# Kernel tuning notes

Measured on AMD Instinct MI355X. Metric: run time of the kernel, lower is better.

The kernel has to match this reference:

```python
import jax, jax.numpy as jnp
import numpy as np

DIM = 2048
NUM_HEADS = 8
HEAD_DIM = DIM // NUM_HEADS
BATCH = 16384
EPS = 1e-5


def setup_inputs() -> dict:
    key = jax.random.key(0)
    ks = jax.random.split(key, 10)
    s = 1.0 / np.sqrt(DIM)
    inp = {
        "x": jax.random.normal(ks[0], (BATCH, 1, DIM), dtype=jnp.float32),
        "w_q": jax.random.uniform(ks[1], (DIM, DIM), jnp.float32, -s, s),
        "b_q": jax.random.uniform(ks[2], (DIM,), jnp.float32, -s, s),
        "w_k": jax.random.uniform(ks[3], (DIM, DIM), jnp.float32, -s, s),
        "b_k": jax.random.uniform(ks[4], (DIM,), jnp.float32, -s, s),
        "w_v": jax.random.uniform(ks[5], (DIM, DIM), jnp.float32, -s, s),
        "b_v": jax.random.uniform(ks[6], (DIM,), jnp.float32, -s, s),
        "w_o": jax.random.uniform(ks[7], (DIM, DIM), jnp.float32, -s, s),
        "b_o": jax.random.uniform(ks[8], (DIM,), jnp.float32, -s, s),
        "ln_gamma": jnp.ones((DIM,), jnp.float32),
        "ln_beta": jnp.zeros((DIM,), jnp.float32),
    }
    return inp


def _layer_norm(x, gamma, beta):
    mean = jnp.mean(x, axis=-1, keepdims=True)
    var = jnp.mean(jnp.square(x - mean), axis=-1, keepdims=True)
    return (x - mean) * jax.lax.rsqrt(var + EPS) * gamma + beta


def reference(x, w_q, b_q, w_k, b_k, w_v, b_v, w_o, b_o, ln_gamma, ln_beta):
    # x: (B, 1, D). Dropout is identity (eval mode).
    residual = x
    h = _layer_norm(x, ln_gamma, ln_beta)
    q = h @ w_q.T + b_q  # (B, 1, D)
    k = h @ w_k.T + b_k
    v = h @ w_v.T + b_v
    B = x.shape[0]
    # (B, H, 1, hd)
    qh = q.reshape(B, 1, NUM_HEADS, HEAD_DIM).transpose(0, 2, 1, 3)
    kh = k.reshape(B, 1, NUM_HEADS, HEAD_DIM).transpose(0, 2, 1, 3)
    vh = v.reshape(B, 1, NUM_HEADS, HEAD_DIM).transpose(0, 2, 1, 3)
    scale = HEAD_DIM ** -0.5
    # (B, H, 1, 1); with seq_len=1 softmax is trivially 1, but keep the math faithful
    scores = jnp.einsum("bhqd,bhkd->bhqk", qh, kh) * scale
    probs = jax.nn.softmax(scores, axis=-1)
    attn = jnp.einsum("bhqk,bhkd->bhqd", probs, vh)  # (B, H, 1, hd)
    attn = attn.transpose(0, 2, 1, 3).reshape(B, 1, DIM)
    out = attn @ w_o.T + b_o
    out = out + residual
    return out[:, 0, :]  # squeeze seq dim -> (B, D)
```

## Files before the change

### kernel.cpp

```cpp
#include <hip/hip_runtime.h>
#include <hip/hip_bf16.h>
#include <cstdint>

#define D_MODEL 2048
#define N_BATCH 16384

typedef __attribute__((ext_vector_type(8))) __bf16 bf16x8;
typedef __attribute__((ext_vector_type(4))) float f32x4;

__device__ __forceinline__ unsigned short f2bf(float f) {
    unsigned int u = __builtin_bit_cast(unsigned int, f);
    u += 0x7fffu + ((u >> 16) & 1u);
    return (unsigned short)(u >> 16);
}

__global__ __launch_bounds__(256) void prep_kernel(
    const float* __restrict__ w_v, const float* __restrict__ w_o,
    const float* __restrict__ b_v, const float* __restrict__ b_o,
    unsigned short* __restrict__ wvT, unsigned short* __restrict__ woB,
    float* __restrict__ b_c)
{
    __shared__ float tile[32][33];
    const int b = blockIdx.x;
    const int t = threadIdx.x;
    if (b < 4096) {
        const int nb = 64;
        const int k0 = (b % nb) * 32;
        const int j0 = (b / nb) * 32;
        const int tx = t & 31, ty0 = t >> 5;
        #pragma unroll
        for (int i = 0; i < 32; i += 8) {
            int j = ty0 + i;
            tile[j][tx] = w_v[(long)(j0 + j) * D_MODEL + k0 + tx];
        }
        __syncthreads();
        #pragma unroll
        for (int i = 0; i < 32; i += 8) {
            int kk = ty0 + i;
            wvT[(long)(k0 + kk) * D_MODEL + j0 + tx] = f2bf(tile[tx][kk]);
        }
    } else if (b < 6144) {
        long i = ((long)(b - 4096) * 256 + t) * 8;
        const float4* in4 = reinterpret_cast<const float4*>(w_o + i);
        float4 a = in4[0], bb = in4[1];
        union { unsigned short u[8]; uint4 v; } o;
        o.u[0] = f2bf(a.x); o.u[1] = f2bf(a.y); o.u[2] = f2bf(a.z); o.u[3] = f2bf(a.w);
        o.u[4] = f2bf(bb.x); o.u[5] = f2bf(bb.y); o.u[6] = f2bf(bb.z); o.u[7] = f2bf(bb.w);
        *reinterpret_cast<uint4*>(woB + i) = o.v;
    } else {
        const int n = b - 6144;
        const float4* w4 = reinterpret_cast<const float4*>(w_o + (long)n * D_MODEL);
        const float4* v4 = reinterpret_cast<const float4*>(b_v);
        float4 a = w4[t], bb = w4[256 + t], va = v4[t], vb = v4[256 + t];
        float s = a.x*va.x + a.y*va.y + a.z*va.z + a.w*va.w
                + bb.x*vb.x + bb.y*vb.y + bb.z*vb.z + bb.w*vb.w;
        #pragma unroll
        for (int off = 32; off; off >>= 1) s += __shfl_xor(s, off);
        float* red = &tile[0][0];
        const int lane = t & 63, wid = t >> 6;
        if (lane == 0) red[wid] = s;
        __syncthreads();
        if (t == 0) b_c[n] = red[0] + red[1] + red[2] + red[3] + b_o[n];
    }
}

__global__ __launch_bounds__(256) void lnwc_kernel(
    const unsigned short* __restrict__ A, const unsigned short* __restrict__ B,
    unsigned short* __restrict__ C,
    const float* __restrict__ x, const float* __restrict__ gamma,
    const float* __restrict__ beta, unsigned short* __restrict__ h)
{
    __shared__ __align__(16) unsigned short Alds[128 * 32];
    __shared__ __align__(16) unsigned short Blds[128 * 32];
    const int t = threadIdx.x;

    if (blockIdx.x < 256) {
        const int K = D_MODEL, N = D_MODEL;
        int wg = blockIdx.x;
        wg = (wg & 7) * 32 + (wg >> 3);
        const int bm = wg >> 4, bn = wg & 15;

        const int lane = t & 63, wid = t >> 6;
        const int wr = wid >> 1, wc = wid & 1;

        f32x4 acc[4][4];
        #pragma unroll
        for (int i = 0; i < 4; i++)
            #pragma unroll
            for (int j = 0; j < 4; j++) acc[i][j] = (f32x4){0.f, 0.f, 0.f, 0.f};

        const long Abase = (long)bm * 128 * K;
        const long Bbase = (long)bn * 128 * K;
        const int ci0 = wid * 64 + lane;
        const int ci1 = 256 + ci0;
        const int r0 = ci0 >> 2, c0 = (ci0 & 3) * 8;
        const int r1 = ci1 >> 2, c1 = (ci1 & 3) * 8;

        const int arow = wr * 64 + (lane & 15);
        const int brow = wc * 64 + (lane & 15);
        const int koff = (lane >> 4) * 8;

        for (int k0 = 0; k0 < K; k0 += 32) {
            __builtin_amdgcn_global_load_lds(
                (const __attribute__((address_space(1))) void*)(A + Abase + (long)r0 * K + k0 + c0),
                (__attribute__((address_space(3))) void*)(Alds + wid * 512), 16, 0, 0);
            __builtin_amdgcn_global_load_lds(
                (const __attribute__((address_space(1))) void*)(A + Abase + (long)r1 * K + k0 + c1),
                (__attribute__((address_space(3))) void*)(Alds + 2048 + wid * 512), 16, 0, 0);
            __builtin_amdgcn_global_load_lds(
                (const __attribute__((address_space(1))) void*)(B + Bbase + (long)r0 * K + k0 + c0),
                (__attribute__((address_space(3))) void*)(Blds + wid * 512), 16, 0, 0);
            __builtin_amdgcn_global_load_lds(
                (const __attribute__((address_space(1))) void*)(B + Bbase + (long)r1 * K + k0 + c1),
                (__attribute__((address_space(3))) void*)(Blds + 2048 + wid * 512), 16, 0, 0);
            __syncthreads();

            bf16x8 af[4], bfr[4];
            #pragma unroll
            for (int m = 0; m < 4; m++)
                af[m] = *reinterpret_cast<const bf16x8*>(&Alds[(arow + m * 16) * 32 + koff]);
            #pragma unroll
            for (int n = 0; n < 4; n++)
                bfr[n] = *reinterpret_cast<const bf16x8*>(&Blds[(brow + n * 16) * 32 + koff]);
            #pragma unroll
            for (int m = 0; m < 4; m++)
                #pragma unroll
                for (int n = 0; n < 4; n++)
                    acc[m][n] = __builtin_amdgcn_mfma_f32_16x16x32_bf16(af[m], bfr[n], acc[m][n], 0, 0, 0);
            __syncthreads();
        }

        const int crow0 = bm * 128 + wr * 64 + ((lane >> 4) << 2);
        const int ccol0 = bn * 128 + wc * 64 + (lane & 15);
        #pragma unroll
        for (int m = 0; m < 4; m++)
            #pragma unroll
            for (int j = 0; j < 4; j++) {
                const long r = crow0 + m * 16 + j;
                #pragma unroll
                for (int n = 0; n < 4; n++)
                    C[r * N + ccol0 + n * 16] = f2bf(acc[m][n][j]);
            }
    } else {
        const int row = blockIdx.x - 256;
        const float4* x4 = reinterpret_cast<const float4*>(x + (long)row * D_MODEL);
        float4 a = x4[t];
        float4 b = x4[256 + t];
        float s  = a.x + a.y + a.z + a.w + b.x + b.y + b.z + b.w;
        float ss = a.x*a.x + a.y*a.y + a.z*a.z + a.w*a.w
                 + b.x*b.x + b.y*b.y + b.z*b.z + b.w*b.w;
        #pragma unroll
        for (int off = 32; off; off >>= 1) {
            s  += __shfl_xor(s, off);
            ss += __shfl_xor(ss, off);
        }
        float* red = reinterpret_cast<float*>(Alds);
        const int lane = t & 63, wid = t >> 6;
        if (lane == 0) { red[wid*2] = s; red[wid*2+1] = ss; }
        __syncthreads();
        s  = red[0] + red[2] + red[4] + red[6];
        ss = red[1] + red[3] + red[5] + red[7];
        const float mean = s * (1.0f / D_MODEL);
        const float var  = ss * (1.0f / D_MODEL) - mean * mean;
        const float inv  = rsqrtf(var + 1e-5f);

        const float4* g4  = reinterpret_cast<const float4*>(gamma);
        const float4* be4 = reinterpret_cast<const float4*>(beta);
        ushort4* h4 = reinterpret_cast<ushort4*>(h + (long)row * D_MODEL);
        {
            float4 g = g4[t], be = be4[t];
            ushort4 o;
            o.x = f2bf((a.x - mean) * inv * g.x + be.x);
            o.y = f2bf((a.y - mean) * inv * g.y + be.y);
            o.z = f2bf((a.z - mean) * inv * g.z + be.z);
            o.w = f2bf((a.w - mean) * inv * g.w + be.w);
            h4[t] = o;
        }
        {
            float4 g = g4[256 + t], be = be4[256 + t];
            ushort4 o;
            o.x = f2bf((b.x - mean) * inv * g.x + be.x);
            o.y = f2bf((b.y - mean) * inv * g.y + be.y);
            o.z = f2bf((b.z - mean) * inv * g.z + be.z);
            o.w = f2bf((b.w - mean) * inv * g.w + be.w);
            h4[256 + t] = o;
        }
    }
}

#define GLL(src, dst) __builtin_amdgcn_global_load_lds( \
    (const __attribute__((address_space(1))) void*)(src), \
    (__attribute__((address_space(3))) void*)(dst), 16, 0, 0)
#define WAITV4() do { asm volatile("s_waitcnt vmcnt(4)" ::: "memory"); \
                      __builtin_amdgcn_sched_barrier(0); } while (0)
#define WAITV0() do { asm volatile("s_waitcnt vmcnt(0)" ::: "memory"); \
                      __builtin_amdgcn_sched_barrier(0); } while (0)

__global__ __launch_bounds__(512, 2) void gemm_bt_8ph(
    const unsigned short* __restrict__ A, const unsigned short* __restrict__ B,
    float* __restrict__ C, const float* __restrict__ bias,
    const float* __restrict__ resid, int M, int N, int K)
{
    __shared__ __align__(16) char ldsb[131072];

    const int nBN = N >> 8;
    int wg = blockIdx.x;
    const int cpx = gridDim.x >> 3;
    wg = (wg & 7) * cpx + (wg >> 3);
    const int bm = wg / nBN, bn = wg % nBN;

    const int t = threadIdx.x;
    const int lane = t & 63, wid = t >> 6;
    const int wr = wid >> 2;
    const int wc = wid & 3;

    const long Kl = K;
    const int tr = t >> 3;
    const int c8 = ((t & 7) ^ (tr & 7)) * 8;
    const unsigned short* As = A + (long)(bm * 256 + tr) * Kl + c8;
    const unsigned short* Bs = B + (long)(bn * 256 + tr) * Kl + c8;

#define ST_A(buf, half, kcol) do { \
    const unsigned short* s_ = As + (half) * 128 * Kl + (kcol); \
    char* d_ = ldsb + (buf) * 65536 + (half) * 16384 + t * 16; \
    GLL(s_, d_); GLL(s_ + 64 * Kl, d_ + 8192); } while (0)
#define ST_B(buf, half, kcol) do { \
    const unsigned short* s_ = Bs + (half) * 128 * Kl + (kcol); \
    char* d_ = ldsb + (buf) * 65536 + 32768 + (half) * 16384 + t * 16; \
    GLL(s_, d_); GLL(s_ + 64 * Kl, d_ + 8192); } while (0)

    const int l15 = lane & 15, l4 = lane >> 4;
    const int swz0 = ((l4)     ^ (l15 & 7)) << 4;
    const int swz1 = ((4 + l4) ^ (l15 & 7)) << 4;
    const int aOff = wr * 16384 + l15 * 128;
    const int bOff = 32768 + (wc >> 1) * 16384 + ((wc & 1) * 64 + l15) * 128;

#define LDV(off) (*reinterpret_cast<const bf16x8*>(ldsb + (off)))
#define RD_A(buf, mh) do { \
    _Pragma("unroll") for (int mi = 0; mi < 4; ++mi) \
        af[mi][0] = LDV((buf) * 65536 + aOff + ((mh) * 4 + mi) * 2048 + swz0); \
    _Pragma("unroll") for (int mi = 0; mi < 4; ++mi) \
        af[mi][1] = LDV((buf) * 65536 + aOff + ((mh) * 4 + mi) * 2048 + swz1); } while (0)
#define RD_B0(buf) do { \
    _Pragma("unroll") for (int nj = 0; nj < 2; ++nj) \
        b0[nj][0] = LDV((buf) * 65536 + bOff + nj * 2048 + swz0); \
    _Pragma("unroll") for (int nj = 0; nj < 2; ++nj) \
        b0[nj][1] = LDV((buf) * 65536 + bOff + nj * 2048 + swz1); } while (0)
#define RD_B1(buf) do { \
    _Pragma("unroll") for (int nj = 0; nj < 2; ++nj) \
        b1[nj][0] = LDV((buf) * 65536 + bOff + (2 + nj) * 2048 + swz0); \
    _Pragma("unroll") for (int nj = 0; nj < 2; ++nj) \
        b1[nj][1] = LDV((buf) * 65536 + bOff + (2 + nj) * 2048 + swz1); } while (0)

#define MMQ(mh, nh, BQ) do { \
    __builtin_amdgcn_s_setprio(1); \
    _Pragma("unroll") for (int kk = 0; kk < 2; ++kk) \
    _Pragma("unroll") for (int mi = 0; mi < 4; ++mi) \
    _Pragma("unroll") for (int nj = 0; nj < 2; ++nj) \
        acc[(mh) * 4 + mi][(nh) * 2 + nj] = __builtin_amdgcn_mfma_f32_16x16x32_bf16( \
            af[mi][kk], BQ[nj][kk], acc[(mh) * 4 + mi][(nh) * 2 + nj], 0, 0, 0); \
    __builtin_amdgcn_s_setprio(0); } while (0)
#define ENDP() __builtin_amdgcn_s_barrier()

    bf16x8 af[4][2], b0[2][2], b1[2][2];
    f32x4 acc[8][4];
    #pragma unroll
    for (int i = 0; i < 8; i++)
        #pragma unroll
        for (int j = 0; j < 4; j++) acc[i][j] = (f32x4){0.f, 0.f, 0.f, 0.f};

    const int NI = K >> 7;

    ST_A(0, 0, 0); ST_A(0, 1, 0); ST_B(0, 0, 0); ST_B(0, 1, 0);
    ST_B(1, 0, 64); ST_A(1, 0, 64);
    WAITV4();
    __builtin_amdgcn_s_barrier();

    for (int i = 0; i < NI; ++i) {
        const int kcA1 = (i << 7) + 64;
        const int kcN0 = (i << 7) + 128;
        const int kcN1 = (i << 7) + 192;
        const bool more = (i + 1 < NI);

        RD_A(0, 0); RD_B0(0);
        ST_A(1, 1, kcA1);
        MMQ(0, 0, b0); ENDP();
        RD_B1(0);
        ST_B(1, 1, kcA1);
        MMQ(0, 1, b1); ENDP();
        RD_A(0, 1);
        if (more) ST_B(0, 0, kcN0);
        MMQ(1, 0, b0); ENDP();
        if (more) ST_A(0, 0, kcN0);
        MMQ(1, 1, b1);
        if (more) { WAITV4(); } else { WAITV0(); }
        ENDP();
        RD_A(1, 0); RD_B0(1);
        if (more) ST_A(0, 1, kcN0);
        MMQ(0, 0, b0); ENDP();
        RD_B1(1);
        if (more) ST_B(0, 1, kcN0);
        MMQ(0, 1, b1); ENDP();
        RD_A(1, 1);
        if (more) ST_B(1, 0, kcN1);
        MMQ(1, 0, b0); ENDP();
        if (more) ST_A(1, 0, kcN1);
        MMQ(1, 1, b1);
        if (more) { WAITV4(); }
        ENDP();
    }
#undef ST_A
#undef ST_B
#undef RD_A
#undef RD_B0
#undef RD_B1
#undef MMQ
#undef ENDP
#undef LDV

    const int crow0 = bm * 256 + wr * 128 + l4 * 4;
    const int ccol0 = bn * 256 + wc * 64 + l15;
    #pragma unroll
    for (int m = 0; m < 8; m++)
        #pragma unroll
        for (int j = 0; j < 4; j++) {
            const long r = crow0 + m * 16 + j;
            float* crow = C + r * N;
            const float* rrow = resid + r * N;
            #pragma unroll
            for (int n = 0; n < 4; n++) {
                const int col = ccol0 + n * 16;
                crow[col] = acc[m][n][j] + bias[col] + rrow[col];
            }
        }
}

extern "C" void kernel_launch(void* const* d_in, const int* in_sizes, int n_in,
                              void* d_out, int out_size, void* d_ws, size_t ws_size,
                              hipStream_t stream) {
    const float* x     = (const float*)d_in[0];
    const float* w_v   = (const float*)d_in[5];
    const float* b_v   = (const float*)d_in[6];
    const float* w_o   = (const float*)d_in[7];
    const float* b_o   = (const float*)d_in[8];
    const float* gamma = (const float*)d_in[9];
    const float* beta  = (const float*)d_in[10];
    float* out = (float*)d_out;

    char* ws = (char*)d_ws;
    unsigned short* h   = (unsigned short*)(ws);
    unsigned short* wvT = (unsigned short*)(ws + 67108864L);
    unsigned short* woB = (unsigned short*)(ws + 67108864L + 8388608L);
    unsigned short* Wc  = (unsigned short*)(ws + 67108864L + 2 * 8388608L);
    float*          b_c = (float*)(ws + 67108864L + 3 * 8388608L);

    prep_kernel<<<8192, 256, 0, stream>>>(w_v, w_o, b_v, b_o, wvT, woB, b_c);
    lnwc_kernel<<<256 + N_BATCH, 256, 0, stream>>>(woB, wvT, Wc, x, gamma, beta, h);
    gemm_bt_8ph<<<(N_BATCH / 256) * (D_MODEL / 256), 512, 0, stream>>>(
        h, Wc, out, b_c, x, N_BATCH, D_MODEL, D_MODEL);
}
```

Baseline: 228.6 us.

## Make GEMM persistent over two tiles and fuse w_o bf16 cast into bias prep

The main GEMM now launches 256 workgroups, each computing two 256x256 output tiles. The first k-slices of the second tile are prefetched into LDS before the first tile's epilogue runs, so its global loads overlap the output stores. The prep kernel drops its separate w_o conversion blocks and writes the bf16 copy of w_o from the row-dot-product blocks, which already read that row, removing a duplicate read of w_o. The change also removes the MFMA setprio calls and hoists the bias loads. The risks are a tail imbalance with fewer workgroups and a hardcoded tile mapping that assumes these exact dimensions.

```diff
diff --git a/kernel.cpp b/kernel.cpp
--- a/kernel.cpp
+++ b/kernel.cpp
@@ -39,19 +39,22 @@
             int kk = ty0 + i;
             wvT[(long)(k0 + kk) * D_MODEL + j0 + tx] = f2bf(tile[tx][kk]);
         }
-    } else if (b < 6144) {
-        long i = ((long)(b - 4096) * 256 + t) * 8;
-        const float4* in4 = reinterpret_cast<const float4*>(w_o + i);
-        float4 a = in4[0], bb = in4[1];
-        union { unsigned short u[8]; uint4 v; } o;
-        o.u[0] = f2bf(a.x); o.u[1] = f2bf(a.y); o.u[2] = f2bf(a.z); o.u[3] = f2bf(a.w);
-        o.u[4] = f2bf(bb.x); o.u[5] = f2bf(bb.y); o.u[6] = f2bf(bb.z); o.u[7] = f2bf(bb.w);
-        *reinterpret_cast<uint4*>(woB + i) = o.v;
     } else {
-        const int n = b - 6144;
+        const int n = b - 4096;
         const float4* w4 = reinterpret_cast<const float4*>(w_o + (long)n * D_MODEL);
         const float4* v4 = reinterpret_cast<const float4*>(b_v);
         float4 a = w4[t], bb = w4[256 + t], va = v4[t], vb = v4[256 + t];
+        unsigned short* orow = woB + (long)n * D_MODEL;
+        {
+            ushort4 o;
+            o.x = f2bf(a.x); o.y = f2bf(a.y); o.z = f2bf(a.z); o.w = f2bf(a.w);
+            *reinterpret_cast<ushort4*>(orow + t * 4) = o;
+        }
+        {
+            ushort4 o;
+            o.x = f2bf(bb.x); o.y = f2bf(bb.y); o.z = f2bf(bb.z); o.w = f2bf(bb.w);
+            *reinterpret_cast<ushort4*>(orow + 1024 + t * 4) = o;
+        }
         float s = a.x*va.x + a.y*va.y + a.z*va.z + a.w*va.w
                 + bb.x*vb.x + bb.y*vb.y + bb.z*vb.z + bb.w*vb.w;
         #pragma unroll
@@ -203,12 +206,6 @@
 {
     __shared__ __align__(16) char ldsb[131072];
 
-    const int nBN = N >> 8;
-    int wg = blockIdx.x;
-    const int cpx = gridDim.x >> 3;
-    wg = (wg & 7) * cpx + (wg >> 3);
-    const int bm = wg / nBN, bn = wg % nBN;
-
     const int t = threadIdx.x;
     const int lane = t & 63, wid = t >> 6;
     const int wr = wid >> 2;
@@ -217,23 +214,23 @@
     const long Kl = K;
     const int tr = t >> 3;
     const int c8 = ((t & 7) ^ (tr & 7)) * 8;
-    const unsigned short* As = A + (long)(bm * 256 + tr) * Kl + c8;
-    const unsigned short* Bs = B + (long)(bn * 256 + tr) * Kl + c8;
-
-#define ST_A(buf, half, kcol) do { \
-    const unsigned short* s_ = As + (half) * 128 * Kl + (kcol); \
-    char* d_ = ldsb + (buf) * 65536 + (half) * 16384 + t * 16; \
-    GLL(s_, d_); GLL(s_ + 64 * Kl, d_ + 8192); } while (0)
-#define ST_B(buf, half, kcol) do { \
-    const unsigned short* s_ = Bs + (half) * 128 * Kl + (kcol); \
-    char* d_ = ldsb + (buf) * 65536 + 32768 + (half) * 16384 + t * 16; \
-    GLL(s_, d_); GLL(s_ + 64 * Kl, d_ + 8192); } while (0)
 
     const int l15 = lane & 15, l4 = lane >> 4;
     const int swz0 = ((l4)     ^ (l15 & 7)) << 4;
     const int swz1 = ((4 + l4) ^ (l15 & 7)) << 4;
     const int aOff = wr * 16384 + l15 * 128;
     const int bOff = 32768 + (wc >> 1) * 16384 + ((wc & 1) * 64 + l15) * 128;
+
+    const int wgs = (blockIdx.x & 7) * 32 + (blockIdx.x >> 3);
+
+#define ST_A(P, buf, half, kcol) do { \
+    const unsigned short* s_ = (P) + (half) * 128 * Kl + (kcol); \
+    char* d_ = ldsb + (buf) * 65536 + (half) * 16384 + t * 16; \
+    GLL(s_, d_); GLL(s_ + 64 * Kl, d_ + 8192); } while (0)
+#define ST_B(P, buf, half, kcol) do { \
+    const unsigned short* s_ = (P) + (half) * 128 * Kl + (kcol); \
+    char* d_ = ldsb + (buf) * 65536 + 32768 + (half) * 16384 + t * 16; \
+    GLL(s_, d_); GLL(s_ + 64 * Kl, d_ + 8192); } while (0)
 
 #define LDV(off) (*reinterpret_cast<const bf16x8*>(ldsb + (off)))
 #define RD_A(buf, mh) do { \
@@ -253,61 +250,112 @@
         b1[nj][1] = LDV((buf) * 65536 + bOff + (2 + nj) * 2048 + swz1); } while (0)
 
 #define MMQ(mh, nh, BQ) do { \
-    __builtin_amdgcn_s_setprio(1); \
     _Pragma("unroll") for (int kk = 0; kk < 2; ++kk) \
     _Pragma("unroll") for (int mi = 0; mi < 4; ++mi) \
     _Pragma("unroll") for (int nj = 0; nj < 2; ++nj) \
         acc[(mh) * 4 + mi][(nh) * 2 + nj] = __builtin_amdgcn_mfma_f32_16x16x32_bf16( \
             af[mi][kk], BQ[nj][kk], acc[(mh) * 4 + mi][(nh) * 2 + nj], 0, 0, 0); \
-    __builtin_amdgcn_s_setprio(0); } while (0)
+    } while (0)
 #define ENDP() __builtin_amdgcn_s_barrier()
 
     bf16x8 af[4][2], b0[2][2], b1[2][2];
     f32x4 acc[8][4];
-    #pragma unroll
-    for (int i = 0; i < 8; i++)
-        #pragma unroll
-        for (int j = 0; j < 4; j++) acc[i][j] = (f32x4){0.f, 0.f, 0.f, 0.f};
-
     const int NI = K >> 7;
 
-    ST_A(0, 0, 0); ST_A(0, 1, 0); ST_B(0, 0, 0); ST_B(0, 1, 0);
-    ST_B(1, 0, 64); ST_A(1, 0, 64);
-    WAITV4();
-    __builtin_amdgcn_s_barrier();
-
-    for (int i = 0; i < NI; ++i) {
-        const int kcA1 = (i << 7) + 64;
-        const int kcN0 = (i << 7) + 128;
-        const int kcN1 = (i << 7) + 192;
-        const bool more = (i + 1 < NI);
-
-        RD_A(0, 0); RD_B0(0);
-        ST_A(1, 1, kcA1);
-        MMQ(0, 0, b0); ENDP();
-        RD_B1(0);
-        ST_B(1, 1, kcA1);
-        MMQ(0, 1, b1); ENDP();
-        RD_A(0, 1);
-        if (more) ST_B(0, 0, kcN0);
-        MMQ(1, 0, b0); ENDP();
-        if (more) ST_A(0, 0, kcN0);
-        MMQ(1, 1, b1);
-        if (more) { WAITV4(); } else { WAITV0(); }
-        ENDP();
-        RD_A(1, 0); RD_B0(1);
-        if (more) ST_A(0, 1, kcN0);
-        MMQ(0, 0, b0); ENDP();
-        RD_B1(1);
-        if (more) ST_B(0, 1, kcN0);
-        MMQ(0, 1, b1); ENDP();
-        RD_A(1, 1);
-        if (more) ST_B(1, 0, kcN1);
-        MMQ(1, 0, b0); ENDP();
-        if (more) ST_A(1, 0, kcN1);
-        MMQ(1, 1, b1);
-        if (more) { WAITV4(); }
-        ENDP();
+    {
+        const int bm0 = wgs >> 3, bn0 = wgs & 7;
+        const unsigned short* As = A + (long)(bm0 * 256 + tr) * Kl + c8;
+        const unsigned short* Bs = B + (long)(bn0 * 256 + tr) * Kl + c8;
+        ST_A(As, 0, 0, 0); ST_A(As, 0, 1, 0); ST_B(Bs, 0, 0, 0); ST_B(Bs, 0, 1, 0);
+        ST_B(Bs, 1, 0, 64); ST_A(As, 1, 0, 64);
+    }
+
+    #pragma unroll 1
+    for (int tile = 0; tile < 2; ++tile) {
+        const int wg = wgs + tile * 256;
+        const int bm = wg >> 3, bn = wg & 7;
+        const unsigned short* As = A + (long)(bm * 256 + tr) * Kl + c8;
+        const unsigned short* Bs = B + (long)(bn * 256 + tr) * Kl + c8;
+
+        #pragma unroll
+        for (int i = 0; i < 8; i++)
+            #pragma unroll
+            for (int j = 0; j < 4; j++) acc[i][j] = (f32x4){0.f, 0.f, 0.f, 0.f};
+
+        WAITV4();
+        __builtin_amdgcn_s_barrier();
+
+        for (int i = 0; i < NI; ++i) {
+            const int kcA1 = (i << 7) + 64;
+            const int kcN0 = (i << 7) + 128;
+            const int kcN1 = (i << 7) + 192;
+            const bool more = (i + 1 < NI);
+
+            RD_A(0, 0); RD_B0(0);
+            ST_A(As, 1, 1, kcA1);
+            MMQ(0, 0, b0); ENDP();
+
+            RD_B1(0);
+            ST_B(Bs, 1, 1, kcA1);
+            MMQ(0, 1, b1); ENDP();
+
+            RD_A(0, 1);
+            if (more) ST_B(Bs, 0, 0, kcN0);
+            MMQ(1, 0, b0); ENDP();
+
+            if (more) ST_A(As, 0, 0, kcN0);
+            MMQ(1, 1, b1);
+            if (more) { WAITV4(); } else { WAITV0(); }
+            ENDP();
+
+            RD_A(1, 0); RD_B0(1);
+            if (more) ST_A(As, 0, 1, kcN0);
+            MMQ(0, 0, b0); ENDP();
+
+            RD_B1(1);
+            if (more) ST_B(Bs, 0, 1, kcN0);
+            MMQ(0, 1, b1); ENDP();
+
+            RD_A(1, 1);
+            if (more) ST_B(Bs, 1, 0, kcN1);
+            MMQ(1, 0, b0); ENDP();
+
+            if (more) ST_A(As, 1, 0, kcN1);
+            MMQ(1, 1, b1);
+            if (more) { WAITV4(); }
+            ENDP();
+        }
+
+        if (tile == 0) {
+            const int wg1 = wgs + 256;
+            const int bm1 = wg1 >> 3, bn1 = wg1 & 7;
+            const unsigned short* As1 = A + (long)(bm1 * 256 + tr) * Kl + c8;
+            const unsigned short* Bs1 = B + (long)(bn1 * 256 + tr) * Kl + c8;
+            ST_A(As1, 0, 0, 0); ST_A(As1, 0, 1, 0);
+            ST_B(Bs1, 0, 0, 0); ST_B(Bs1, 0, 1, 0);
+            ST_B(Bs1, 1, 0, 64); ST_A(As1, 1, 0, 64);
+        }
+
+        {
+            const int crow0 = bm * 256 + wr * 128 + l4 * 4;
+            const int ccol0 = bn * 256 + wc * 64 + l15;
+            float bias4[4];
+            #pragma unroll
+            for (int n = 0; n < 4; n++) bias4[n] = bias[ccol0 + n * 16];
+            #pragma unroll
+            for (int m = 0; m < 8; m++)
+                #pragma unroll
+                for (int j = 0; j < 4; j++) {
+                    const long r = crow0 + m * 16 + j;
+                    float* crow = C + r * N;
+                    const float* rrow = resid + r * N;
+                    #pragma unroll
+                    for (int n = 0; n < 4; n++) {
+                        const int col = ccol0 + n * 16;
+                        crow[col] = acc[m][n][j] + bias4[n] + rrow[col];
+                    }
+                }
+        }
     }
 #undef ST_A
 #undef ST_B
@@ -317,22 +365,6 @@
 #undef MMQ
 #undef ENDP
 #undef LDV
-
-    const int crow0 = bm * 256 + wr * 128 + l4 * 4;
-    const int ccol0 = bn * 256 + wc * 64 + l15;
-    #pragma unroll
-    for (int m = 0; m < 8; m++)
-        #pragma unroll
-        for (int j = 0; j < 4; j++) {
-            const long r = crow0 + m * 16 + j;
-            float* crow = C + r * N;
-            const float* rrow = resid + r * N;
-            #pragma unroll
-            for (int n = 0; n < 4; n++) {
-                const int col = ccol0 + n * 16;
-                crow[col] = acc[m][n][j] + bias[col] + rrow[col];
-            }
-        }
 }
 
 extern "C" void kernel_launch(void* const* d_in, const int* in_sizes, int n_in,
@@ -354,8 +386,8 @@
     unsigned short* Wc  = (unsigned short*)(ws + 67108864L + 2 * 8388608L);
     float*          b_c = (float*)(ws + 67108864L + 3 * 8388608L);
 
-    prep_kernel<<<8192, 256, 0, stream>>>(w_v, w_o, b_v, b_o, wvT, woB, b_c);
+    prep_kernel<<<6144, 256, 0, stream>>>(w_v, w_o, b_v, b_o, wvT, woB, b_c);
     lnwc_kernel<<<256 + N_BATCH, 256, 0, stream>>>(woB, wvT, Wc, x, gamma, beta, h);
-    gemm_bt_8ph<<<(N_BATCH / 256) * (D_MODEL / 256), 512, 0, stream>>>(
+    gemm_bt_8ph<<<256, 512, 0, stream>>>(
         h, Wc, out, b_c, x, N_BATCH, D_MODEL, D_MODEL);
 }
```

Result: slower. 235.6 us (+3.1%).
